# Optimization experiments

Hardware: AMD Instinct MI355X
Metric: run time of the kernel (lower is better)

## Reference

```python
import jax, jax.numpy as jnp
import numpy as np

N = 1_000_000
D = 128
NUM_CLASSES = 1000


def setup_inputs() -> dict:
    key = jax.random.key(0)
    k1, k2 = jax.random.split(key)
    embeddings = jax.random.normal(k1, (N, D), dtype=jnp.float32)
    labels = jax.random.randint(k2, (N,), 0, NUM_CLASSES, dtype=jnp.int64)
    return {"embeddings": embeddings, "labels": labels}


def reference(embeddings, labels):
    # Per-class mean via one-pass segment sums (equivalent to the torch
    # per-unique-label masked-mean loop, since all classes are present).
    sums = jax.ops.segment_sum(embeddings, labels, num_segments=NUM_CLASSES)  # [C, D]
    counts = jax.ops.segment_sum(
        jnp.ones((embeddings.shape[0],), dtype=embeddings.dtype), labels,
        num_segments=NUM_CLASSES)  # [C]
    class_means = sums / counts[:, None]  # [C, D]
    # torch.var default is unbiased (ddof=1)
    variance = jnp.var(class_means, axis=0, ddof=1).mean()
    return -variance
```

## Files before the change

### kernel.cpp

```cpp
#include <hip/hip_runtime.h>
#include <stdint.h>

#define NROWS 1000000
#define DDIM  128
#define NCLS  1000

#define WS_HIST   0
#define WS_START  1000
#define WS_CURSOR 2001
#define WS_SORTED 4096
#define WS_GMEAN  1004096
#define WS_ACC    1132096

__global__ void zero_kernel(int* __restrict__ hist, float* __restrict__ acc) {
    int i = blockIdx.x * 256 + threadIdx.x;
    if (i < NCLS) hist[i] = 0;
    if (i == 0) acc[0] = 0.0f;
}

__global__ __launch_bounds__(256) void hist_kernel(const int* __restrict__ labels,
                                                   int* __restrict__ hist) {
    __shared__ int lh[NCLS];
    for (int i = threadIdx.x; i < NCLS; i += 256) lh[i] = 0;
    __syncthreads();
    for (int r = blockIdx.x * 256 + threadIdx.x; r < NROWS; r += 256 * 256)
        atomicAdd(&lh[labels[r]], 1);
    __syncthreads();
    for (int i = threadIdx.x; i < NCLS; i += 256) {
        int v = lh[i];
        if (v) atomicAdd(&hist[i], v);
    }
}

__global__ __launch_bounds__(1024) void scan_kernel(const int* __restrict__ hist,
                                                    int* __restrict__ start,
                                                    int* __restrict__ cursor) {
    __shared__ int sc[1024];
    const int tid = threadIdx.x;
    int v = (tid < NCLS) ? hist[tid] : 0;
    sc[tid] = v;
    __syncthreads();
    for (int off = 1; off < 1024; off <<= 1) {
        int t = (tid >= off) ? sc[tid - off] : 0;
        __syncthreads();
        sc[tid] += t;
        __syncthreads();
    }
    if (tid < NCLS) {
        start[tid + 1] = sc[tid];
        cursor[tid]    = sc[tid] - v;
    }
    if (tid == 0) start[0] = 0;
}

__global__ __launch_bounds__(256) void scatter_kernel(const int* __restrict__ labels,
                                                      int* __restrict__ cursor,
                                                      int* __restrict__ sorted_idx) {
    for (int r = blockIdx.x * 256 + threadIdx.x; r < NROWS; r += 1024 * 256) {
        int lbl = labels[r];
        int pos = atomicAdd(&cursor[lbl], 1);
        sorted_idx[pos] = r;
    }
}

__global__ __launch_bounds__(512) void gather_sum_kernel(
        const float* __restrict__ emb, const int* __restrict__ start,
        const int* __restrict__ sorted_idx, float* __restrict__ gmean) {
    const float2* emb2 = (const float2*)emb;
    const int c    = blockIdx.x;
    const int w    = threadIdx.x >> 6;
    const int lane = threadIdx.x & 63;

    const int a = start[c];
    const int m = start[c + 1] - a;
    const int lo = a + (int)(((long long)m * w) >> 3);
    const int hi = a + (int)(((long long)m * (w + 1)) >> 3);

    float accx = 0.0f, accy = 0.0f;
    int i = lo;
    for (; i + 64 <= hi; i += 64) {
        int idx = sorted_idx[i + lane];
        #pragma unroll
        for (int jj = 0; jj < 64; jj += 8) {
            float2 vv[8];
            #pragma unroll
            for (int u = 0; u < 8; u++) {
                int r = __shfl(idx, jj + u);
                vv[u] = emb2[(size_t)r * 64 + lane];
            }
            #pragma unroll
            for (int u = 0; u < 8; u++) { accx += vv[u].x; accy += vv[u].y; }
        }
    }
    int n = hi - i;
    if (n > 0) {
        int idx = sorted_idx[i + (lane < n ? lane : n - 1)];
        for (int j = 0; j < n; j++) {
            int r = __shfl(idx, j);
            float2 v = emb2[(size_t)r * 64 + lane];
            accx += v.x; accy += v.y;
        }
    }

    __shared__ float red[8][DDIM];
    red[w][2 * lane]     = accx;
    red[w][2 * lane + 1] = accy;
    __syncthreads();
    if (threadIdx.x < DDIM) {
        float s = 0.0f;
        #pragma unroll
        for (int k = 0; k < 8; k++) s += red[k][threadIdx.x];
        gmean[c * DDIM + threadIdx.x] = (m > 0) ? (s / (float)m) : 0.0f;
    }
}

__global__ __launch_bounds__(256) void var_kernel(const float* __restrict__ gmean,
                                                  float* __restrict__ acc) {
    const int d = blockIdx.x;
    float s1 = 0.0f, s2 = 0.0f;
    for (int c = threadIdx.x; c < NCLS; c += 256) {
        float mv = gmean[c * DDIM + d];
        s1 += mv;
        s2 += mv * mv;
    }
    #pragma unroll
    for (int off = 32; off; off >>= 1) {
        s1 += __shfl_down(s1, off);
        s2 += __shfl_down(s2, off);
    }
    __shared__ float p1[4], p2[4];
    int wave = threadIdx.x >> 6, lane = threadIdx.x & 63;
    if (lane == 0) { p1[wave] = s1; p2[wave] = s2; }
    __syncthreads();
    if (threadIdx.x == 0) {
        float t1 = p1[0] + p1[1] + p1[2] + p1[3];
        float t2 = p2[0] + p2[1] + p2[2] + p2[3];
        float var = (t2 - t1 * t1 / (float)NCLS) / (float)(NCLS - 1);
        atomicAdd(acc, var);
    }
}

__global__ void final_kernel(const float* __restrict__ acc, float* __restrict__ out) {
    out[0] = -acc[0] / (float)DDIM;
}

extern "C" void kernel_launch(void* const* d_in, const int* in_sizes, int n_in,
                              void* d_out, int out_size, void* d_ws, size_t ws_size,
                              hipStream_t stream) {
    const float* emb    = (const float*)d_in[0];
    const int*   labels = (const int*)d_in[1];
    int*   wsi    = (int*)d_ws;
    float* wsf    = (float*)d_ws;
    int*   hist   = wsi + WS_HIST;
    int*   start  = wsi + WS_START;
    int*   cursor = wsi + WS_CURSOR;
    int*   sorted = wsi + WS_SORTED;
    float* gmean  = wsf + WS_GMEAN;
    float* acc    = wsf + WS_ACC;
    float* out    = (float*)d_out;

    hipLaunchKernelGGL(zero_kernel, dim3(4), dim3(256), 0, stream, hist, acc);
    hipLaunchKernelGGL(hist_kernel, dim3(256), dim3(256), 0, stream, labels, hist);
    hipLaunchKernelGGL(scan_kernel, dim3(1), dim3(1024), 0, stream, hist, start, cursor);
    hipLaunchKernelGGL(scatter_kernel, dim3(1024), dim3(256), 0, stream, labels, cursor, sorted);
    hipLaunchKernelGGL(gather_sum_kernel, dim3(NCLS), dim3(512), 0, stream,
                       emb, start, sorted, gmean);
    hipLaunchKernelGGL(var_kernel, dim3(DDIM), dim3(256), 0, stream, gmean, acc);
    hipLaunchKernelGGL(final_kernel, dim3(1), dim3(1), 0, stream, acc, out);
}
```

Baseline: 931.3 us.

## Widen gather to float4 nontemporal loads and drop atomics in histogram and variance

The gather-sum kernel now loads 16-byte float4 chunks with nontemporal hints, so each wave covers two rows per load instruction. Each half-wave handles one row, and the shared reduction grows to 16 partials. The histogram writes per-block partial counts that the scan kernel sums, which removes the zero kernel and the global atomics. Variance per dimension is stored and reduced by a 64-thread final kernel instead of a float atomicAdd, and the scatter grid shrinks to 256 blocks. Together these target the dominant random row-gather bandwidth and remove one launch, at the cost of a serial 64-way sum in the scan.

Measured after the change: 835.5 us. 10.3% less time.

```diff
diff --git a/kernel.cpp b/kernel.cpp
--- a/kernel.cpp
+++ b/kernel.cpp
@@ -4,40 +4,38 @@
 #define NROWS 1000000
 #define DDIM  128
 #define NCLS  1000
+#define HBLK  64
+#define RPH   (NROWS / HBLK)
 
-#define WS_HIST   0
-#define WS_START  1000
-#define WS_CURSOR 2001
-#define WS_SORTED 4096
-#define WS_GMEAN  1004096
-#define WS_ACC    1132096
+typedef float f4 __attribute__((ext_vector_type(4)));
 
-__global__ void zero_kernel(int* __restrict__ hist, float* __restrict__ acc) {
-    int i = blockIdx.x * 256 + threadIdx.x;
-    if (i < NCLS) hist[i] = 0;
-    if (i == 0) acc[0] = 0.0f;
+#define WS_PART   0
+#define WS_START  64000
+#define WS_CURSOR 65008
+#define WS_SORTED 66048
+#define WS_GMEAN  1066048
+#define WS_VARD   1194048
+
+__global__ __launch_bounds__(1024) void hist_kernel(const int* __restrict__ labels,
+                                                    int* __restrict__ part) {
+    __shared__ int lh[NCLS];
+    for (int i = threadIdx.x; i < NCLS; i += 1024) lh[i] = 0;
+    __syncthreads();
+    const int b = blockIdx.x;
+    for (int r = b * RPH + threadIdx.x; r < (b + 1) * RPH; r += 1024)
+        atomicAdd(&lh[labels[r]], 1);
+    __syncthreads();
+    for (int i = threadIdx.x; i < NCLS; i += 1024) part[b * NCLS + i] = lh[i];
 }
 
-__global__ __launch_bounds__(256) void hist_kernel(const int* __restrict__ labels,
-                                                   int* __restrict__ hist) {
-    __shared__ int lh[NCLS];
-    for (int i = threadIdx.x; i < NCLS; i += 256) lh[i] = 0;
-    __syncthreads();
-    for (int r = blockIdx.x * 256 + threadIdx.x; r < NROWS; r += 256 * 256)
-        atomicAdd(&lh[labels[r]], 1);
-    __syncthreads();
-    for (int i = threadIdx.x; i < NCLS; i += 256) {
-        int v = lh[i];
-        if (v) atomicAdd(&hist[i], v);
-    }
-}
-
-__global__ __launch_bounds__(1024) void scan_kernel(const int* __restrict__ hist,
+__global__ __launch_bounds__(1024) void scan_kernel(const int* __restrict__ part,
                                                     int* __restrict__ start,
                                                     int* __restrict__ cursor) {
     __shared__ int sc[1024];
     const int tid = threadIdx.x;
-    int v = (tid < NCLS) ? hist[tid] : 0;
+    int v = 0;
+    if (tid < NCLS)
+        for (int b = 0; b < HBLK; b++) v += part[b * NCLS + tid];
     sc[tid] = v;
     __syncthreads();
     for (int off = 1; off < 1024; off <<= 1) {
@@ -56,7 +54,7 @@
 __global__ __launch_bounds__(256) void scatter_kernel(const int* __restrict__ labels,
                                                       int* __restrict__ cursor,
                                                       int* __restrict__ sorted_idx) {
-    for (int r = blockIdx.x * 256 + threadIdx.x; r < NROWS; r += 1024 * 256) {
+    for (int r = blockIdx.x * 256 + threadIdx.x; r < NROWS; r += 256 * 256) {
         int lbl = labels[r];
         int pos = atomicAdd(&cursor[lbl], 1);
         sorted_idx[pos] = r;
@@ -66,56 +64,59 @@
 __global__ __launch_bounds__(512) void gather_sum_kernel(
         const float* __restrict__ emb, const int* __restrict__ start,
         const int* __restrict__ sorted_idx, float* __restrict__ gmean) {
-    const float2* emb2 = (const float2*)emb;
+    const f4* emb4 = (const f4*)emb;
     const int c    = blockIdx.x;
     const int w    = threadIdx.x >> 6;
     const int lane = threadIdx.x & 63;
+    const int half = lane >> 5;
+    const int q    = lane & 31;
 
     const int a = start[c];
     const int m = start[c + 1] - a;
     const int lo = a + (int)(((long long)m * w) >> 3);
     const int hi = a + (int)(((long long)m * (w + 1)) >> 3);
 
-    float accx = 0.0f, accy = 0.0f;
+    f4 acc = {0.0f, 0.0f, 0.0f, 0.0f};
     int i = lo;
     for (; i + 64 <= hi; i += 64) {
         int idx = sorted_idx[i + lane];
         #pragma unroll
-        for (int jj = 0; jj < 64; jj += 8) {
-            float2 vv[8];
+        for (int jj = 0; jj < 64; jj += 16) {
+            f4 vv[8];
             #pragma unroll
             for (int u = 0; u < 8; u++) {
-                int r = __shfl(idx, jj + u);
-                vv[u] = emb2[(size_t)r * 64 + lane];
+                int r = __shfl(idx, jj + 2 * u + half);
+                vv[u] = __builtin_nontemporal_load(&emb4[(size_t)r * 32 + q]);
             }
             #pragma unroll
-            for (int u = 0; u < 8; u++) { accx += vv[u].x; accy += vv[u].y; }
+            for (int u = 0; u < 8; u++) acc += vv[u];
         }
     }
     int n = hi - i;
     if (n > 0) {
         int idx = sorted_idx[i + (lane < n ? lane : n - 1)];
-        for (int j = 0; j < n; j++) {
-            int r = __shfl(idx, j);
-            float2 v = emb2[(size_t)r * 64 + lane];
-            accx += v.x; accy += v.y;
+        for (int j = 0; j < n; j += 2) {
+            if (j + half < n) {
+                int r = __shfl(idx, j + half);
+                acc += __builtin_nontemporal_load(&emb4[(size_t)r * 32 + q]);
+            }
         }
     }
 
-    __shared__ float red[8][DDIM];
-    red[w][2 * lane]     = accx;
-    red[w][2 * lane + 1] = accy;
+    __shared__ float red[16 * DDIM];
+    f4* red4 = (f4*)red;
+    red4[(w * 2 + half) * 32 + q] = acc;
     __syncthreads();
     if (threadIdx.x < DDIM) {
         float s = 0.0f;
         #pragma unroll
-        for (int k = 0; k < 8; k++) s += red[k][threadIdx.x];
+        for (int k = 0; k < 16; k++) s += red[k * DDIM + threadIdx.x];
         gmean[c * DDIM + threadIdx.x] = (m > 0) ? (s / (float)m) : 0.0f;
     }
 }
 
 __global__ __launch_bounds__(256) void var_kernel(const float* __restrict__ gmean,
-                                                  float* __restrict__ acc) {
+                                                  float* __restrict__ var_d) {
     const int d = blockIdx.x;
     float s1 = 0.0f, s2 = 0.0f;
     for (int c = threadIdx.x; c < NCLS; c += 256) {
@@ -135,13 +136,16 @@
     if (threadIdx.x == 0) {
         float t1 = p1[0] + p1[1] + p1[2] + p1[3];
         float t2 = p2[0] + p2[1] + p2[2] + p2[3];
-        float var = (t2 - t1 * t1 / (float)NCLS) / (float)(NCLS - 1);
-        atomicAdd(acc, var);
+        var_d[d] = (t2 - t1 * t1 / (float)NCLS) / (float)(NCLS - 1);
     }
 }
 
-__global__ void final_kernel(const float* __restrict__ acc, float* __restrict__ out) {
-    out[0] = -acc[0] / (float)DDIM;
+__global__ __launch_bounds__(64) void final_kernel(const float* __restrict__ var_d,
+                                                   float* __restrict__ out) {
+    float s = var_d[threadIdx.x] + var_d[threadIdx.x + 64];
+    #pragma unroll
+    for (int off = 32; off; off >>= 1) s += __shfl_down(s, off);
+    if (threadIdx.x == 0) out[0] = -s / (float)DDIM;
 }
 
 extern "C" void kernel_launch(void* const* d_in, const int* in_sizes, int n_in,
@@ -151,20 +155,19 @@
     const int*   labels = (const int*)d_in[1];
     int*   wsi    = (int*)d_ws;
     float* wsf    = (float*)d_ws;
-    int*   hist   = wsi + WS_HIST;
+    int*   part   = wsi + WS_PART;
     int*   start  = wsi + WS_START;
     int*   cursor = wsi + WS_CURSOR;
     int*   sorted = wsi + WS_SORTED;
     float* gmean  = wsf + WS_GMEAN;
-    float* acc    = wsf + WS_ACC;
+    float* var_d  = wsf + WS_VARD;
     float* out    = (float*)d_out;
 
-    hipLaunchKernelGGL(zero_kernel, dim3(4), dim3(256), 0, stream, hist, acc);
-    hipLaunchKernelGGL(hist_kernel, dim3(256), dim3(256), 0, stream, labels, hist);
-    hipLaunchKernelGGL(scan_kernel, dim3(1), dim3(1024), 0, stream, hist, start, cursor);
-    hipLaunchKernelGGL(scatter_kernel, dim3(1024), dim3(256), 0, stream, labels, cursor, sorted);
+    hipLaunchKernelGGL(hist_kernel, dim3(HBLK), dim3(1024), 0, stream, labels, part);
+    hipLaunchKernelGGL(scan_kernel, dim3(1), dim3(1024), 0, stream, part, start, cursor);
+    hipLaunchKernelGGL(scatter_kernel, dim3(256), dim3(256), 0, stream, labels, cursor, sorted);
     hipLaunchKernelGGL(gather_sum_kernel, dim3(NCLS), dim3(512), 0, stream,
                        emb, start, sorted, gmean);
-    hipLaunchKernelGGL(var_kernel, dim3(DDIM), dim3(256), 0, stream, gmean, acc);
-    hipLaunchKernelGGL(final_kernel, dim3(1), dim3(1), 0, stream, acc, out);
+    hipLaunchKernelGGL(var_kernel, dim3(DDIM), dim3(256), 0, stream, gmean, var_d);
+    hipLaunchKernelGGL(final_kernel, dim3(1), dim3(64), 0, stream, var_d, out);
 }
```
